# Optimization experiments

Hardware: AMD Instinct MI355X
Metric: run time of the kernel (lower is better)

The kernel has to match this reference:

```python
import jax, jax.numpy as jnp
import numpy as np
import math

# ---- module hyperparameters (from init_kwargs) ----
IN_CHANS, OUT_CHANS = 64, 64
NLAT_IN, NLON_IN = 91, 180
NLAT_OUT, NLON_OUT = 91, 180  # same resolution -> longitudinal stride 1
NR, NPHI = 5, 6               # kernel_shape
KSIZE = (NR - 1) * NPHI + 1   # 25 basis functions (1 center + (NR-1)*NPHI ring sectors)
THETA_CUTOFF = 4.0 * math.pi / float(NLAT_OUT - 1)
# latitude support window: basis vanishes for |theta_out - theta_in| > cutoff
_HALF = int(math.ceil(THETA_CUTOFF / (math.pi / (NLAT_IN - 1))))
WIN = 2 * _HALF + 1


def _precompute_psi():
    """Precompute DISCO basis tensor psi (values of the piecewise-linear
    spherical basis functions, weighted by quadrature weights), restricted to
    the latitudinal support window. Returns (psi [K,To,W,P], ti_idx [To,W])."""
    theta_in = np.pi * np.arange(NLAT_IN) / (NLAT_IN - 1)    # equiangular colatitudes
    theta_out = np.pi * np.arange(NLAT_OUT) / (NLAT_OUT - 1)
    phi_in = 2.0 * np.pi * np.arange(NLON_IN) / NLON_IN
    offs = np.arange(-_HALF, _HALF + 1)
    ti_raw = np.arange(NLAT_OUT)[:, None] + offs[None, :]    # [To, W]
    valid = (ti_raw >= 0) & (ti_raw < NLAT_IN)
    ti_idx = np.clip(ti_raw, 0, NLAT_IN - 1)
    to = theta_out[:, None, None]                            # [To,1,1]
    ti = theta_in[ti_idx][:, :, None]                        # [To,W,1]
    ph = phi_in[None, None, :]                               # [1,1,P]
    # coordinates of input point in frame where the output point (theta_out, 0)
    # is rotated to the north pole (rotation by -theta_out about y-axis)
    xx = np.cos(to) * np.sin(ti) * np.cos(ph) - np.sin(to) * np.cos(ti)
    yy = np.sin(ti) * np.sin(ph)
    zz = np.sin(to) * np.sin(ti) * np.cos(ph) + np.cos(to) * np.cos(ti)
    r = np.arccos(np.clip(zz, -1.0, 1.0))                    # great-circle distance
    phi = np.mod(np.arctan2(yy, xx), 2.0 * np.pi)            # azimuth around output point
    dr = THETA_CUTOFF / (NR - 1)
    dphi = 2.0 * np.pi / NPHI
    inside = (r <= THETA_CUTOFF) & valid[:, :, None]
    psi = np.zeros((KSIZE,) + r.shape, dtype=np.float64)
    # k = 0: isotropic center hat
    psi[0] = np.where(inside, np.maximum(0.0, 1.0 - r / dr), 0.0)
    # rings ir = 1..NR-1, azimuthal sectors ip = 0..NPHI-1 (periodic hat in phi)
    for ir in range(1, NR):
        rad = np.maximum(0.0, 1.0 - np.abs(r - ir * dr) / dr)
        for ip in range(NPHI):
            dp = np.abs(np.mod(phi - ip * dphi + np.pi, 2.0 * np.pi) - np.pi)
            ang = np.maximum(0.0, 1.0 - dp / dphi)
            psi[1 + (ir - 1) * NPHI + ip] = np.where(inside, rad * ang, 0.0)
    # fold in equiangular quadrature weights of the input grid
    quad = np.sin(theta_in) * (np.pi / (NLAT_IN - 1)) * (2.0 * np.pi / NLON_IN)
    psi = psi * quad[ti_idx][None, :, :, None]
    return jnp.asarray(psi, dtype=jnp.float32), jnp.asarray(ti_idx, dtype=jnp.int32)


PSI, TI_IDX = _precompute_psi()  # PSI: [K, To, W, P], TI_IDX: [To, W]


def setup_inputs() -> dict:
    key = jax.random.key(0)
    k1, k2 = jax.random.split(key)
    x = jax.random.normal(k1, (2, IN_CHANS, NLAT_IN, NLON_IN), dtype=jnp.float32)
    scale = 1.0 / math.sqrt(IN_CHANS * KSIZE)
    weight = scale * jax.random.normal(k2, (OUT_CHANS, IN_CHANS, KSIZE), dtype=jnp.float32)
    return {"x": x, "weight": weight}


def reference(x, weight):
    # DISCO S2 conv: out[b,o,to,q] = sum_{c,k} w[o,c,k] * sum_{ti,p} psi[k,to,ti,(p-q) mod P] * x[b,c,ti,p]
    # The longitudinal shift is a circular cross-correlation -> evaluate via rFFT.
    x = x.astype(jnp.float32)  # wrapper casts to float32 around the conv
    xw = x[:, :, TI_IDX, :]                          # [B,C,To,W,P] latitudinal gather
    Xf = jnp.fft.rfft(xw, axis=-1)                   # [B,C,To,W,F]
    Pf = jnp.fft.rfft(PSI, axis=-1)                  # [K,To,W,F]
    # correlation: FFT(z) = conj(FFT(psi)) * FFT(x), contracting the lat window
    Zf = jnp.einsum('ktwf,bctwf->bcktf', jnp.conj(Pf), Xf)   # [B,C,K,To,F]
    Of = jnp.einsum('ock,bcktf->botf', weight.astype(Zf.dtype), Zf)
    out = jnp.fft.irfft(Of, n=NLON_IN, axis=-1)      # [B,Cout,To,P]
    return out.astype(x.dtype)
```

## Files before the change

kernel.cpp:

```cpp
#include <hip/hip_runtime.h>
#include <math.h>
#include <string.h>

#define NLAT 91
#define NLON 180
#define NCH  64
#define KSZ  25
#define NW   9
#define HALF 4
#define NB   2
#define NPK  16
#define CG   8
#define PPB  (NPK / CG)
#define THREADS 192
#define EUNIT 384
#define ECAP  131072
#define UCAP  512
#define XSCAP 2560
#define LCAP  1024

#define KOFF_OFF  0
#define ROW_OFF   9472
#define UNITS_OFF 22784
#define ENTS_OFF  30976
#define BLOB_MAX  (ENTS_OFF + (size_t)ECAP * 8)

#ifndef M_PI
#define M_PI 3.14159265358979323846
#endif

typedef unsigned int u32;

static int build_tables(unsigned char* blob, int* ne_out)
{
#pragma clang fp contract(off)
    int*  koff  = (int*)(blob + KOFF_OFF);
    int4* rowi  = (int4*)(blob + ROW_OFF);
    u32*  units = (u32*)(blob + UNITS_OFF);
    u32*  ents  = (u32*)(blob + ENTS_OFF);

    static double sth[NLAT], cth[NLAT], cphv[NLON], sphv[NLON];
    for (int t = 0; t < NLAT; t++) {
        double th = (M_PI * (double)t) / 90.0;
        sth[t] = sin(th); cth[t] = cos(th);
    }
    for (int q = 0; q < NLON; q++) {
        double ph = (2.0 * M_PI * (double)q) / 180.0;
        cphv[q] = cos(ph); sphv[q] = sin(ph);
    }
    const double cutoff = (4.0 * M_PI) / 90.0;
    const double dr     = cutoff / 4.0;
    const double dphi   = (2.0 * M_PI) / 6.0;

    static int   lcnt[KSZ];
    static int   loff_[KSZ][LCAP];
    static float lval[KSZ][LCAP];

    int ne = 0, nu = 0;
    for (int t = 0; t < NLAT; t++) {
        for (int k = 0; k < KSZ; k++) lcnt[k] = 0;
        int dqmin[NW], dqmax[NW];
        for (int w = 0; w < NW; w++) { dqmin[w] = 999; dqmax[w] = -999; }
        for (int w = 0; w < NW; w++) {
            int ti_raw = t - HALF + w;
            int valid = (ti_raw >= 0) && (ti_raw < NLAT);
            int ti = ti_raw < 0 ? 0 : (ti_raw > NLAT - 1 ? NLAT - 1 : ti_raw);
            for (int dq = -89; dq <= 90; dq++) {
                int q = dq < 0 ? dq + NLON : dq;
                double t1 = sth[t] * sth[ti];
                double t2 = t1 * cphv[q];
                double t3 = cth[t] * cth[ti];
                double zz = t2 + t3;
                if (zz > 1.0) zz = 1.0;
                if (zz < -1.0) zz = -1.0;
                double r = acos(zz);
                if (!(valid && (r <= cutoff))) continue;
                if (dq < dqmin[w]) dqmin[w] = dq;
                if (dq > dqmax[w]) dqmax[w] = dq;
                double xx = (cth[t] * sth[ti]) * cphv[q] - sth[t] * cth[ti];
                double yy = sth[ti] * sphv[q];
                double phi = atan2(yy, xx);
                { double m = fmod(phi, 2.0 * M_PI); if (m < 0.0) m += 2.0 * M_PI; phi = m; }
                double quad = sth[ti] * (M_PI / 90.0) * ((2.0 * M_PI) / 180.0);
                double v0 = fmax(0.0, 1.0 - r / dr);
                float f0 = (float)(v0 * quad);
                int pid = w * 512 + (dq + 128);
                if (f0 != 0.f && lcnt[0] < LCAP) {
                    loff_[0][lcnt[0]] = pid; lval[0][lcnt[0]] = f0; lcnt[0]++;
                }
                for (int ir = 1; ir < 5; ir++) {
                    double rad = fmax(0.0, 1.0 - fabs(r - ir * dr) / dr);
                    for (int ip = 0; ip < 6; ip++) {
                        double a = (phi - ip * dphi) + M_PI;
                        double m = fmod(a, 2.0 * M_PI);
                        if (m < 0.0) m += 2.0 * M_PI;
                        double dp = fabs(m - M_PI);
                        double ang = fmax(0.0, 1.0 - dp / dphi);
                        float f = (float)((rad * ang) * quad);
                        int k = 1 + (ir - 1) * 6 + ip;
                        if (f != 0.f && lcnt[k] < LCAP) {
                            loff_[k][lcnt[k]] = pid; lval[k][lcnt[k]] = f; lcnt[k]++;
                        }
                    }
                }
            }
        }
        int rb = 0, base[NW];
        for (int w = 0; w < NW; w++) {
            int len = (dqmin[w] <= dqmax[w]) ? (NLON + dqmax[w] - dqmin[w]) : 0;
            if (rb + len > XSCAP) len = XSCAP - rb;
            int tw = t - HALF + w;
            int ti = tw < 0 ? 0 : (tw > NLAT - 1 ? NLAT - 1 : tw);
            base[w] = rb;
            rowi[t * NW + w] = make_int4(rb, len, (dqmin[w] <= dqmax[w]) ? dqmin[w] : 0, ti);
            rb += len;
        }
        int tBase = ne;
        for (int k = 0; k < KSZ; k++) {
            koff[t * (KSZ + 1) + k] = ne;
            for (int i = 0; i < lcnt[k] && ne < ECAP; i++) {
                int pid = loff_[k][i];
                int w = pid >> 9, dq = (pid & 511) - 128;
                u32 off = (u32)(base[w] + (dq - rowi[t * NW + w].z));
                ents[2 * ne] = off;
                float fv = lval[k][i];
                u32 fb; memcpy(&fb, &fv, 4);
                ents[2 * ne + 1] = fb;
                ne++;
            }
            while (((ne - koff[t * (KSZ + 1) + k]) & 3) && ne < ECAP) {
                ents[2 * ne] = 0; ents[2 * ne + 1] = 0; ne++;
            }
        }
        koff[t * (KSZ + 1) + KSZ] = ne;
        for (int e0 = tBase; e0 < ne; e0 += EUNIT) {
            int e1 = e0 + EUNIT < ne ? e0 + EUNIT : ne;
            int kb = 0;
            while (kb < KSZ &&
                   !(koff[t * (KSZ + 1) + kb] <= e0 && e0 < koff[t * (KSZ + 1) + kb + 1]))
                kb++;
            if (nu < UCAP) {
                units[nu * 4 + 0] = (u32)t;
                units[nu * 4 + 1] = (u32)e0;
                units[nu * 4 + 2] = (u32)e1;
                units[nu * 4 + 3] = (u32)kb;
                nu++;
            }
        }
    }
    *ne_out = ne;
    return nu;
}

struct GInit {
    unsigned char* blob;
    int nu, ne;
    size_t bytes;
    GInit() {
        static unsigned char storage[BLOB_MAX];
        nu = build_tables(storage, &ne);
        bytes = ENTS_OFF + (size_t)ne * 8;
        unsigned char* p = nullptr;
        if (hipHostMalloc((void**)&p, bytes) == hipSuccess && p) {
            memcpy(p, storage, bytes);
            blob = p;
        } else {
            blob = storage;
        }
    }
};
static GInit g_init;

__global__ __launch_bounds__(THREADS) void pack_x(const float* __restrict__ x,
                                                  float4* __restrict__ xp4)
{
    int t = blockIdx.x, cp = blockIdx.y, b = blockIdx.z;
    int p = threadIdx.x;
    if (p >= NLON) return;
    int c0 = cp * 4;
    float4 v;
    v.x = x[((size_t)(b * NCH + c0 + 0) * NLAT + t) * NLON + p];
    v.y = x[((size_t)(b * NCH + c0 + 1) * NLAT + t) * NLON + p];
    v.z = x[((size_t)(b * NCH + c0 + 2) * NLAT + t) * NLON + p];
    v.w = x[((size_t)(b * NCH + c0 + 3) * NLAT + t) * NLON + p];
    xp4[((size_t)(b * NPK + cp) * NLAT + t) * NLON + p] = v;
}

__global__ void pack_w(const float* __restrict__ wgt, float4* __restrict__ wt2)
{
    int i = blockIdx.x * blockDim.x + threadIdx.x;
    if (i >= NPK * KSZ * NCH) return;
    int cp = i / (KSZ * NCH);
    int rem = i - cp * (KSZ * NCH);
    int k = rem / NCH;
    int o = rem - k * NCH;
    float4 v;
    v.x = wgt[((size_t)o * NCH + cp * 4 + 0) * KSZ + k];
    v.y = wgt[((size_t)o * NCH + cp * 4 + 1) * KSZ + k];
    v.z = wgt[((size_t)o * NCH + cp * 4 + 2) * KSZ + k];
    v.w = wgt[((size_t)o * NCH + cp * 4 + 3) * KSZ + k];
    wt2[i] = v;
}

__global__ __launch_bounds__(THREADS, 3) void disco_fused(
    const float4* __restrict__ xp4, const float4* __restrict__ wt2,
    const uint2* __restrict__ ents, const int* __restrict__ koffG,
    const int4* __restrict__ rowinfoG, const uint4* __restrict__ units,
    float* __restrict__ out)
{
    uint4 uu = units[blockIdx.x];
    int t    = __builtin_amdgcn_readfirstlane((int)uu.x);
    int eBeg = __builtin_amdgcn_readfirstlane((int)uu.y);
    int eEnd = __builtin_amdgcn_readfirstlane((int)uu.z);
    int kBeg = __builtin_amdgcn_readfirstlane((int)uu.w);
    if (eBeg >= eEnd) return;
    int cg = blockIdx.y, b = blockIdx.z;
    int tid = threadIdx.x;
    int p = tid < NLON ? tid : NLON - 1;
    bool act = tid < NLON;

    __shared__ float4 xs[XSCAP];
    const int* ko = koffG + t * (KSZ + 1);
    const int4* ri9 = rowinfoG + t * NW;

    float acc[NCH];
#pragma unroll
    for (int o = 0; o < NCH; o++) acc[o] = 0.f;

    for (int pk = 0; pk < PPB; pk++) {
        int cp = cg * PPB + pk;
        __syncthreads();
#pragma unroll
        for (int w = 0; w < NW; w++) {
            int4 ri = ri9[w];
            const float4* src = xp4 + ((size_t)(b * NPK + cp) * NLAT + ri.w) * NLON;
            for (int j = tid; j < ri.y; j += THREADS) {
                int s = j + ri.z;
                if (s < 0) s += NLON;
                if (s >= NLON) s -= NLON;
                xs[ri.x + j] = src[s];
            }
        }
        __syncthreads();

        int e = eBeg, k = kBeg;
        while (e < eEnd) {
            int kend = ko[k + 1];
            if (kend > eEnd) kend = eEnd;
            if (kend > e) {
                float z00=0.f,z01=0.f,z02=0.f,z03=0.f;
                float z10=0.f,z11=0.f,z12=0.f,z13=0.f;
                float z20=0.f,z21=0.f,z22=0.f,z23=0.f;
                float z30=0.f,z31=0.f,z32=0.f,z33=0.f;
                for (; e < kend; e += 4) {
                    const uint4* e4 = (const uint4*)(ents + e);
                    uint4 A = e4[0], B = e4[1];
                    float4 x0 = xs[A.x + p];
                    float4 x1 = xs[A.z + p];
                    float4 x2 = xs[B.x + p];
                    float4 x3 = xs[B.z + p];
                    float v0 = __uint_as_float(A.y), v1 = __uint_as_float(A.w);
                    float v2 = __uint_as_float(B.y), v3 = __uint_as_float(B.w);
                    z00 = fmaf(v0, x0.x, z00); z01 = fmaf(v0, x0.y, z01);
                    z02 = fmaf(v0, x0.z, z02); z03 = fmaf(v0, x0.w, z03);
                    z10 = fmaf(v1, x1.x, z10); z11 = fmaf(v1, x1.y, z11);
                    z12 = fmaf(v1, x1.z, z12); z13 = fmaf(v1, x1.w, z13);
                    z20 = fmaf(v2, x2.x, z20); z21 = fmaf(v2, x2.y, z21);
                    z22 = fmaf(v2, x2.z, z22); z23 = fmaf(v2, x2.w, z23);
                    z30 = fmaf(v3, x3.x, z30); z31 = fmaf(v3, x3.y, z31);
                    z32 = fmaf(v3, x3.z, z32); z33 = fmaf(v3, x3.w, z33);
                }
                float zc0 = (z00 + z10) + (z20 + z30);
                float zc1 = (z01 + z11) + (z21 + z31);
                float zc2 = (z02 + z12) + (z22 + z32);
                float zc3 = (z03 + z13) + (z23 + z33);
                const float4* wk = wt2 + ((size_t)cp * KSZ + k) * NCH;
#pragma unroll
                for (int o = 0; o < NCH; o++) {
                    float4 w4 = wk[o];
                    acc[o] = fmaf(w4.w, zc3, fmaf(w4.z, zc2,
                             fmaf(w4.y, zc1, fmaf(w4.x, zc0, acc[o]))));
                }
            }
            k++;
            if (k >= KSZ) break;
        }
    }

    if (act) {
        float* op = out + ((size_t)b * NCH * NLAT * NLON) + (size_t)t * NLON + p;
#pragma unroll
        for (int o = 0; o < NCH; o++)
            atomicAdd(op + (size_t)o * (NLAT * NLON), acc[o]);
    }
}

extern "C" void kernel_launch(void* const* d_in, const int* in_sizes, int n_in,
                              void* d_out, int out_size, void* d_ws, size_t ws_size,
                              hipStream_t stream)
{
    const float* x   = (const float*)d_in[0];
    const float* wgt = (const float*)d_in[1];
    char* ws = (char*)d_ws;

    size_t cur = 0;
    auto alloc = [&](size_t bytes) { size_t o = cur; cur = (cur + bytes + 255) & ~(size_t)255; return o; };
    size_t blob_off = alloc(BLOB_MAX);
    size_t xp4_off  = alloc((size_t)NB * NPK * NLAT * NLON * 16);
    size_t wt2_off  = alloc((size_t)NPK * KSZ * NCH * 16);

    unsigned char* d_blob = (unsigned char*)(ws + blob_off);
    float4*        xp4    = (float4*)(ws + xp4_off);
    float4*        wt2    = (float4*)(ws + wt2_off);

    hipMemcpyAsync(d_blob, g_init.blob, g_init.bytes, hipMemcpyHostToDevice, stream);
    pack_x<<<dim3(NLAT, NPK, NB), THREADS, 0, stream>>>(x, xp4);
    pack_w<<<(NPK * KSZ * NCH + 255) / 256, 256, 0, stream>>>(wgt, wt2);
    hipMemsetAsync(d_out, 0, (size_t)out_size * 4, stream);

    const uint2* entsD = (const uint2*)(d_blob + ENTS_OFF);
    const int*   koffD = (const int*)(d_blob + KOFF_OFF);
    const int4*  rowD  = (const int4*)(d_blob + ROW_OFF);
    const uint4* unitD = (const uint4*)(d_blob + UNITS_OFF);

    disco_fused<<<dim3(g_init.nu, CG, NB), THREADS, 0, stream>>>(
        xp4, wt2, entsD, koffD, rowD, unitD, (float*)d_out);
}
```

Measured before the change: 407.0 us.

## Pair two entry units per block to share the staged shared-memory input tile

Each block now holds two 192-thread groups, each processing a different entry unit of the same output latitude, while they share one shared-memory load of the latitude window. Units are paired on the host, and an odd trailing unit is split in half so every pair is complete. This halves the redundant global-to-LDS staging per unit and cuts the block count, at the cost of larger blocks. Register pressure rises under the launch-bound occupancy hint of 6, and uneven work between the two halves can leave threads idle.

```diff
diff --git a/kernel.cpp b/kernel.cpp
--- a/kernel.cpp
+++ b/kernel.cpp
@@ -12,17 +12,17 @@
 #define NPK  16
 #define CG   8
 #define PPB  (NPK / CG)
-#define THREADS 192
+#define THREADS 384
 #define EUNIT 384
 #define ECAP  131072
 #define UCAP  512
-#define XSCAP 2560
+#define XSCAP 2496
 #define LCAP  1024
 
 #define KOFF_OFF  0
 #define ROW_OFF   9472
 #define UNITS_OFF 22784
-#define ENTS_OFF  30976
+#define ENTS_OFF  39168
 #define BLOB_MAX  (ENTS_OFF + (size_t)ECAP * 8)
 
 #ifndef M_PI
@@ -56,7 +56,7 @@
     static int   loff_[KSZ][LCAP];
     static float lval[KSZ][LCAP];
 
-    int ne = 0, nu = 0;
+    int ne = 0, nPairs = 0;
     for (int t = 0; t < NLAT; t++) {
         for (int k = 0; k < KSZ; k++) lcnt[k] = 0;
         int dqmin[NW], dqmax[NW];
@@ -133,23 +133,37 @@
             }
         }
         koff[t * (KSZ + 1) + KSZ] = ne;
-        for (int e0 = tBase; e0 < ne; e0 += EUNIT) {
+        int tu[128][2]; int ntu = 0;
+        for (int e0 = tBase; e0 < ne && ntu < 127; e0 += EUNIT) {
             int e1 = e0 + EUNIT < ne ? e0 + EUNIT : ne;
-            int kb = 0;
-            while (kb < KSZ &&
-                   !(koff[t * (KSZ + 1) + kb] <= e0 && e0 < koff[t * (KSZ + 1) + kb + 1]))
-                kb++;
-            if (nu < UCAP) {
-                units[nu * 4 + 0] = (u32)t;
-                units[nu * 4 + 1] = (u32)e0;
-                units[nu * 4 + 2] = (u32)e1;
-                units[nu * 4 + 3] = (u32)kb;
-                nu++;
+            tu[ntu][0] = e0; tu[ntu][1] = e1; ntu++;
+        }
+        if (ntu & 1) {
+            int a = tu[ntu - 1][0], b = tu[ntu - 1][1];
+            int m = a + (((b - a) / 2 + 3) & ~3);
+            if (m > b) m = b;
+            tu[ntu - 1][1] = m;
+            tu[ntu][0] = m; tu[ntu][1] = b;
+            ntu++;
+        }
+        for (int i = 0; i + 1 < ntu; i += 2) {
+            int kb0 = 0, kb1 = 0;
+            while (kb0 < KSZ && !(koff[t * (KSZ + 1) + kb0] <= tu[i][0] &&
+                                  tu[i][0] < koff[t * (KSZ + 1) + kb0 + 1])) kb0++;
+            while (kb1 < KSZ && !(koff[t * (KSZ + 1) + kb1] <= tu[i + 1][0] &&
+                                  tu[i + 1][0] < koff[t * (KSZ + 1) + kb1 + 1])) kb1++;
+            if (nPairs < UCAP) {
+                u32* up = units + nPairs * 8;
+                up[0] = (u32)t;
+                up[1] = (u32)tu[i][0];     up[2] = (u32)tu[i][1];     up[3] = (u32)kb0;
+                up[4] = (u32)tu[i + 1][0]; up[5] = (u32)tu[i + 1][1]; up[6] = (u32)kb1;
+                up[7] = 0;
+                nPairs++;
             }
         }
     }
     *ne_out = ne;
-    return nu;
+    return nPairs;
 }
 
 struct GInit {
@@ -171,8 +185,8 @@
 };
 static GInit g_init;
 
-__global__ __launch_bounds__(THREADS) void pack_x(const float* __restrict__ x,
-                                                  float4* __restrict__ xp4)
+__global__ __launch_bounds__(192) void pack_x(const float* __restrict__ x,
+                                              float4* __restrict__ xp4)
 {
     int t = blockIdx.x, cp = blockIdx.y, b = blockIdx.z;
     int p = threadIdx.x;
@@ -202,22 +216,25 @@
     wt2[i] = v;
 }
 
-__global__ __launch_bounds__(THREADS, 3) void disco_fused(
+__global__ __launch_bounds__(THREADS, 6) void disco_fused(
     const float4* __restrict__ xp4, const float4* __restrict__ wt2,
     const uint2* __restrict__ ents, const int* __restrict__ koffG,
     const int4* __restrict__ rowinfoG, const uint4* __restrict__ units,
     float* __restrict__ out)
 {
-    uint4 uu = units[blockIdx.x];
-    int t    = __builtin_amdgcn_readfirstlane((int)uu.x);
-    int eBeg = __builtin_amdgcn_readfirstlane((int)uu.y);
-    int eEnd = __builtin_amdgcn_readfirstlane((int)uu.z);
-    int kBeg = __builtin_amdgcn_readfirstlane((int)uu.w);
-    if (eBeg >= eEnd) return;
+    const uint4 ua = units[(size_t)blockIdx.x * 2];
+    const uint4 ub = units[(size_t)blockIdx.x * 2 + 1];
+    int tid = threadIdx.x;
+    bool grpB = (tid >= 192);
+    int t    = __builtin_amdgcn_readfirstlane((int)ua.x);
+    int eBeg = __builtin_amdgcn_readfirstlane((int)(grpB ? ub.x : ua.y));
+    int eEnd = __builtin_amdgcn_readfirstlane((int)(grpB ? ub.y : ua.z));
+    int kBeg = __builtin_amdgcn_readfirstlane((int)(grpB ? ub.z : ua.w));
     int cg = blockIdx.y, b = blockIdx.z;
-    int tid = threadIdx.x;
-    int p = tid < NLON ? tid : NLON - 1;
-    bool act = tid < NLON;
+    int lid = grpB ? tid - 192 : tid;
+    int p = lid < NLON ? lid : NLON - 1;
+    bool act = lid < NLON;
+    bool hasWork = eBeg < eEnd;
 
     __shared__ float4 xs[XSCAP];
     const int* ko = koffG + t * (KSZ + 1);
@@ -243,51 +260,53 @@
         }
         __syncthreads();
 
-        int e = eBeg, k = kBeg;
-        while (e < eEnd) {
-            int kend = ko[k + 1];
-            if (kend > eEnd) kend = eEnd;
-            if (kend > e) {
-                float z00=0.f,z01=0.f,z02=0.f,z03=0.f;
-                float z10=0.f,z11=0.f,z12=0.f,z13=0.f;
-                float z20=0.f,z21=0.f,z22=0.f,z23=0.f;
-                float z30=0.f,z31=0.f,z32=0.f,z33=0.f;
-                for (; e < kend; e += 4) {
-                    const uint4* e4 = (const uint4*)(ents + e);
-                    uint4 A = e4[0], B = e4[1];
-                    float4 x0 = xs[A.x + p];
-                    float4 x1 = xs[A.z + p];
-                    float4 x2 = xs[B.x + p];
-                    float4 x3 = xs[B.z + p];
-                    float v0 = __uint_as_float(A.y), v1 = __uint_as_float(A.w);
-                    float v2 = __uint_as_float(B.y), v3 = __uint_as_float(B.w);
-                    z00 = fmaf(v0, x0.x, z00); z01 = fmaf(v0, x0.y, z01);
-                    z02 = fmaf(v0, x0.z, z02); z03 = fmaf(v0, x0.w, z03);
-                    z10 = fmaf(v1, x1.x, z10); z11 = fmaf(v1, x1.y, z11);
-                    z12 = fmaf(v1, x1.z, z12); z13 = fmaf(v1, x1.w, z13);
-                    z20 = fmaf(v2, x2.x, z20); z21 = fmaf(v2, x2.y, z21);
-                    z22 = fmaf(v2, x2.z, z22); z23 = fmaf(v2, x2.w, z23);
-                    z30 = fmaf(v3, x3.x, z30); z31 = fmaf(v3, x3.y, z31);
-                    z32 = fmaf(v3, x3.z, z32); z33 = fmaf(v3, x3.w, z33);
+        if (hasWork) {
+            int e = eBeg, k = kBeg;
+            while (e < eEnd) {
+                int kend = ko[k + 1];
+                if (kend > eEnd) kend = eEnd;
+                if (kend > e) {
+                    float z00=0.f,z01=0.f,z02=0.f,z03=0.f;
+                    float z10=0.f,z11=0.f,z12=0.f,z13=0.f;
+                    float z20=0.f,z21=0.f,z22=0.f,z23=0.f;
+                    float z30=0.f,z31=0.f,z32=0.f,z33=0.f;
+                    for (; e < kend; e += 4) {
+                        const uint4* e4 = (const uint4*)(ents + e);
+                        uint4 A = e4[0], B = e4[1];
+                        float4 x0 = xs[A.x + p];
+                        float4 x1 = xs[A.z + p];
+                        float4 x2 = xs[B.x + p];
+                        float4 x3 = xs[B.z + p];
+                        float v0 = __uint_as_float(A.y), v1 = __uint_as_float(A.w);
+                        float v2 = __uint_as_float(B.y), v3 = __uint_as_float(B.w);
+                        z00 = fmaf(v0, x0.x, z00); z01 = fmaf(v0, x0.y, z01);
+                        z02 = fmaf(v0, x0.z, z02); z03 = fmaf(v0, x0.w, z03);
+                        z10 = fmaf(v1, x1.x, z10); z11 = fmaf(v1, x1.y, z11);
+                        z12 = fmaf(v1, x1.z, z12); z13 = fmaf(v1, x1.w, z13);
+                        z20 = fmaf(v2, x2.x, z20); z21 = fmaf(v2, x2.y, z21);
+                        z22 = fmaf(v2, x2.z, z22); z23 = fmaf(v2, x2.w, z23);
+                        z30 = fmaf(v3, x3.x, z30); z31 = fmaf(v3, x3.y, z31);
+                        z32 = fmaf(v3, x3.z, z32); z33 = fmaf(v3, x3.w, z33);
+                    }
+                    float zc0 = (z00 + z10) + (z20 + z30);
+                    float zc1 = (z01 + z11) + (z21 + z31);
+                    float zc2 = (z02 + z12) + (z22 + z32);
+                    float zc3 = (z03 + z13) + (z23 + z33);
+                    const float4* wk = wt2 + ((size_t)cp * KSZ + k) * NCH;
+#pragma unroll
+                    for (int o = 0; o < NCH; o++) {
+                        float4 w4 = wk[o];
+                        acc[o] = fmaf(w4.w, zc3, fmaf(w4.z, zc2,
+                                 fmaf(w4.y, zc1, fmaf(w4.x, zc0, acc[o]))));
+                    }
                 }
-                float zc0 = (z00 + z10) + (z20 + z30);
-                float zc1 = (z01 + z11) + (z21 + z31);
-                float zc2 = (z02 + z12) + (z22 + z32);
-                float zc3 = (z03 + z13) + (z23 + z33);
-                const float4* wk = wt2 + ((size_t)cp * KSZ + k) * NCH;
-#pragma unroll
-                for (int o = 0; o < NCH; o++) {
-                    float4 w4 = wk[o];
-                    acc[o] = fmaf(w4.w, zc3, fmaf(w4.z, zc2,
-                             fmaf(w4.y, zc1, fmaf(w4.x, zc0, acc[o]))));
-                }
-            }
-            k++;
-            if (k >= KSZ) break;
-        }
-    }
-
-    if (act) {
+                k++;
+                if (k >= KSZ) break;
+            }
+        }
+    }
+
+    if (act && hasWork) {
         float* op = out + ((size_t)b * NCH * NLAT * NLON) + (size_t)t * NLON + p;
 #pragma unroll
         for (int o = 0; o < NCH; o++)
@@ -314,7 +333,7 @@
     float4*        wt2    = (float4*)(ws + wt2_off);
 
     hipMemcpyAsync(d_blob, g_init.blob, g_init.bytes, hipMemcpyHostToDevice, stream);
-    pack_x<<<dim3(NLAT, NPK, NB), THREADS, 0, stream>>>(x, xp4);
+    pack_x<<<dim3(NLAT, NPK, NB), 192, 0, stream>>>(x, xp4);
     pack_w<<<(NPK * KSZ * NCH + 255) / 256, 256, 0, stream>>>(wgt, wt2);
     hipMemsetAsync(d_out, 0, (size_t)out_size * 4, stream);
 
```

Result: slower. 586.8 us (+44.2%).

## Group stencil points by radial/azimuthal cell to share one x load across basis functions

Applied to the files above, without the earlier changes.

Replaces the per-basis-function sparse entry list with a per-point table grouped into 30 (ring, sector) classes. Each point stores up to four hat-function weights, so one shared-memory x load feeds all basis functions that overlap it, and ring accumulators roll through the rings and flush into the output channels. The grid also changes from work units of 384 entries times 8 channel groups to one block per (latitude, channel pack, batch), dropping the unit table. In exchange, each thread holds roughly 50 extra live accumulator registers alongside the 64 output accumulators. The loop is heavily templated and unrolled, and blocks now carry uneven work per latitude.

```diff
diff --git a/kernel.cpp b/kernel.cpp
--- a/kernel.cpp
+++ b/kernel.cpp
@@ -10,20 +10,15 @@
 #define HALF 4
 #define NB   2
 #define NPK  16
-#define CG   8
-#define PPB  (NPK / CG)
 #define THREADS 192
-#define EUNIT 384
-#define ECAP  131072
-#define UCAP  512
-#define XSCAP 2560
-#define LCAP  1024
-
-#define KOFF_OFF  0
-#define ROW_OFF   9472
-#define UNITS_OFF 22784
-#define ENTS_OFF  30976
-#define BLOB_MAX  (ENTS_OFF + (size_t)ECAP * 8)
+#define XSCAP 2496
+#define PCAP  49152
+#define CCAP  2048
+
+#define CLS_OFF   0
+#define ROW_OFF   11520
+#define PSIS_OFF  24832
+#define BLOB_MAX  (PSIS_OFF + (size_t)PCAP * 16 + 64 + (size_t)PCAP * 4)
 
 #ifndef M_PI
 #define M_PI 3.14159265358979323846
@@ -31,13 +26,12 @@
 
 typedef unsigned int u32;
 
-static int build_tables(unsigned char* blob, int* ne_out)
+static int build_tables(unsigned char* blob, size_t* offs_off_out)
 {
 #pragma clang fp contract(off)
-    int*  koff  = (int*)(blob + KOFF_OFF);
-    int4* rowi  = (int4*)(blob + ROW_OFF);
-    u32*  units = (u32*)(blob + UNITS_OFF);
-    u32*  ents  = (u32*)(blob + ENTS_OFF);
+    int*   clsOff = (int*)(blob + CLS_OFF);
+    int4*  rowi   = (int4*)(blob + ROW_OFF);
+    float* psis   = (float*)(blob + PSIS_OFF);
 
     static double sth[NLAT], cth[NLAT], cphv[NLON], sphv[NLON];
     for (int t = 0; t < NLAT; t++) {
@@ -52,15 +46,18 @@
     const double dr     = cutoff / 4.0;
     const double dphi   = (2.0 * M_PI) / 6.0;
 
-    static int   lcnt[KSZ];
-    static int   loff_[KSZ][LCAP];
-    static float lval[KSZ][LCAP];
-
-    int ne = 0, nu = 0;
+    static int   cw[30][CCAP];
+    static int   cdq[30][CCAP];
+    static float cps[30][CCAP][4];
+    static int   ccnt[30];
+    static u32   toffs[PCAP];
+
+    int np = 0;
     for (int t = 0; t < NLAT; t++) {
-        for (int k = 0; k < KSZ; k++) lcnt[k] = 0;
+        for (int c = 0; c < 30; c++) ccnt[c] = 0;
         int dqmin[NW], dqmax[NW];
         for (int w = 0; w < NW; w++) { dqmin[w] = 999; dqmax[w] = -999; }
+
         for (int w = 0; w < NW; w++) {
             int ti_raw = t - HALF + w;
             int valid = (ti_raw >= 0) && (ti_raw < NLAT);
@@ -82,26 +79,51 @@
                 double phi = atan2(yy, xx);
                 { double m = fmod(phi, 2.0 * M_PI); if (m < 0.0) m += 2.0 * M_PI; phi = m; }
                 double quad = sth[ti] * (M_PI / 90.0) * ((2.0 * M_PI) / 180.0);
-                double v0 = fmax(0.0, 1.0 - r / dr);
-                float f0 = (float)(v0 * quad);
-                int pid = w * 512 + (dq + 128);
-                if (f0 != 0.f && lcnt[0] < LCAP) {
-                    loff_[0][lcnt[0]] = pid; lval[0][lcnt[0]] = f0; lcnt[0]++;
+
+                int ir = (int)floor(r / dr);  if (ir > 4) ir = 4; if (ir < 0) ir = 0;
+                int ip = (int)floor(phi / dphi); if (ip > 5) ip = 5; if (ip < 0) ip = 0;
+                int ip1 = (ip + 1) % 6;
+
+                double angL, angH;
+                {
+                    double a = (phi - ip * dphi) + M_PI;
+                    double m = fmod(a, 2.0 * M_PI); if (m < 0.0) m += 2.0 * M_PI;
+                    double dp = fabs(m - M_PI);
+                    angL = fmax(0.0, 1.0 - dp / dphi);
                 }
-                for (int ir = 1; ir < 5; ir++) {
-                    double rad = fmax(0.0, 1.0 - fabs(r - ir * dr) / dr);
-                    for (int ip = 0; ip < 6; ip++) {
-                        double a = (phi - ip * dphi) + M_PI;
-                        double m = fmod(a, 2.0 * M_PI);
-                        if (m < 0.0) m += 2.0 * M_PI;
-                        double dp = fabs(m - M_PI);
-                        double ang = fmax(0.0, 1.0 - dp / dphi);
-                        float f = (float)((rad * ang) * quad);
-                        int k = 1 + (ir - 1) * 6 + ip;
-                        if (f != 0.f && lcnt[k] < LCAP) {
-                            loff_[k][lcnt[k]] = pid; lval[k][lcnt[k]] = f; lcnt[k]++;
-                        }
-                    }
+                {
+                    double a = (phi - ip1 * dphi) + M_PI;
+                    double m = fmod(a, 2.0 * M_PI); if (m < 0.0) m += 2.0 * M_PI;
+                    double dp = fabs(m - M_PI);
+                    angH = fmax(0.0, 1.0 - dp / dphi);
+                }
+                float s0 = 0.f, s1 = 0.f, s2 = 0.f, s3 = 0.f;
+                if (ir == 0) {
+                    double rad0 = fmax(0.0, 1.0 - r / dr);
+                    double rad1 = fmax(0.0, 1.0 - fabs(r - dr) / dr);
+                    s0 = (float)(rad0 * quad);
+                    s1 = (float)((rad1 * angL) * quad);
+                    s2 = (float)((rad1 * angH) * quad);
+                } else if (ir == 4) {
+                    double rad4 = fmax(0.0, 1.0 - fabs(r - 4.0 * dr) / dr);
+                    s0 = (float)((rad4 * angL) * quad);
+                    s1 = (float)((rad4 * angH) * quad);
+                } else {
+                    double radL = fmax(0.0, 1.0 - fabs(r - ir * dr) / dr);
+                    double radH = fmax(0.0, 1.0 - fabs(r - (ir + 1) * dr) / dr);
+                    s0 = (float)((radL * angL) * quad);
+                    s1 = (float)((radL * angH) * quad);
+                    s2 = (float)((radH * angL) * quad);
+                    s3 = (float)((radH * angH) * quad);
+                }
+                if (s0 == 0.f && s1 == 0.f && s2 == 0.f && s3 == 0.f) continue;
+                int cls = ir * 6 + ip;
+                int n = ccnt[cls];
+                if (n < CCAP) {
+                    cw[cls][n] = w; cdq[cls][n] = dq;
+                    cps[cls][n][0] = s0; cps[cls][n][1] = s1;
+                    cps[cls][n][2] = s2; cps[cls][n][3] = s3;
+                    ccnt[cls] = n + 1;
                 }
             }
         }
@@ -115,51 +137,34 @@
             rowi[t * NW + w] = make_int4(rb, len, (dqmin[w] <= dqmax[w]) ? dqmin[w] : 0, ti);
             rb += len;
         }
-        int tBase = ne;
-        for (int k = 0; k < KSZ; k++) {
-            koff[t * (KSZ + 1) + k] = ne;
-            for (int i = 0; i < lcnt[k] && ne < ECAP; i++) {
-                int pid = loff_[k][i];
-                int w = pid >> 9, dq = (pid & 511) - 128;
-                u32 off = (u32)(base[w] + (dq - rowi[t * NW + w].z));
-                ents[2 * ne] = off;
-                float fv = lval[k][i];
-                u32 fb; memcpy(&fb, &fv, 4);
-                ents[2 * ne + 1] = fb;
-                ne++;
+        for (int cls = 0; cls < 30; cls++) {
+            clsOff[t * 31 + cls] = np;
+            for (int i = 0; i < ccnt[cls] && np < PCAP; i++) {
+                int w = cw[cls][i], dq = cdq[cls][i];
+                toffs[np] = (u32)(base[w] + (dq - rowi[t * NW + w].z));
+                psis[4 * np + 0] = cps[cls][i][0];
+                psis[4 * np + 1] = cps[cls][i][1];
+                psis[4 * np + 2] = cps[cls][i][2];
+                psis[4 * np + 3] = cps[cls][i][3];
+                np++;
             }
-            while (((ne - koff[t * (KSZ + 1) + k]) & 3) && ne < ECAP) {
-                ents[2 * ne] = 0; ents[2 * ne + 1] = 0; ne++;
-            }
-        }
-        koff[t * (KSZ + 1) + KSZ] = ne;
-        for (int e0 = tBase; e0 < ne; e0 += EUNIT) {
-            int e1 = e0 + EUNIT < ne ? e0 + EUNIT : ne;
-            int kb = 0;
-            while (kb < KSZ &&
-                   !(koff[t * (KSZ + 1) + kb] <= e0 && e0 < koff[t * (KSZ + 1) + kb + 1]))
-                kb++;
-            if (nu < UCAP) {
-                units[nu * 4 + 0] = (u32)t;
-                units[nu * 4 + 1] = (u32)e0;
-                units[nu * 4 + 2] = (u32)e1;
-                units[nu * 4 + 3] = (u32)kb;
-                nu++;
-            }
-        }
-    }
-    *ne_out = ne;
-    return nu;
+        }
+        clsOff[t * 31 + 30] = np;
+    }
+    size_t offs_off = (PSIS_OFF + (size_t)np * 16 + 63) & ~(size_t)63;
+    memcpy(blob + offs_off, toffs, (size_t)np * 4);
+    *offs_off_out = offs_off;
+    return np;
 }
 
 struct GInit {
     unsigned char* blob;
-    int nu, ne;
-    size_t bytes;
+    int np;
+    size_t bytes, offs_off;
     GInit() {
         static unsigned char storage[BLOB_MAX];
-        nu = build_tables(storage, &ne);
-        bytes = ENTS_OFF + (size_t)ne * 8;
+        np = build_tables(storage, &offs_off);
+        bytes = offs_off + (size_t)np * 4;
         unsigned char* p = nullptr;
         if (hipHostMalloc((void**)&p, bytes) == hipSuccess && p) {
             memcpy(p, storage, bytes);
@@ -171,8 +176,8 @@
 };
 static GInit g_init;
 
-__global__ __launch_bounds__(THREADS) void pack_x(const float* __restrict__ x,
-                                                  float4* __restrict__ xp4)
+__global__ __launch_bounds__(192) void pack_x(const float* __restrict__ x,
+                                              float4* __restrict__ xp4)
 {
     int t = blockIdx.x, cp = blockIdx.y, b = blockIdx.z;
     int p = threadIdx.x;
@@ -202,90 +207,125 @@
     wt2[i] = v;
 }
 
+template<int ROW, int IP>
+__device__ __forceinline__ void runSeg(int sBeg, int sEnd,
+    const u32* __restrict__ offsG, const float4* __restrict__ psisG,
+    const float4* xs, int p,
+    float (&z0)[4], float (&zA)[6][4], float (&zB)[6][4])
+{
+    constexpr int IP1 = (IP + 1) % 6;
+#pragma unroll 2
+    for (int s = sBeg; s < sEnd; ++s) {
+        u32 off = offsG[s];
+        float4 ps = psisG[s];
+        float4 xv = xs[off + p];
+        if (ROW == 0) {
+            z0[0] = fmaf(ps.x, xv.x, z0[0]); z0[1] = fmaf(ps.x, xv.y, z0[1]);
+            z0[2] = fmaf(ps.x, xv.z, z0[2]); z0[3] = fmaf(ps.x, xv.w, z0[3]);
+            zB[IP][0] = fmaf(ps.y, xv.x, zB[IP][0]); zB[IP][1] = fmaf(ps.y, xv.y, zB[IP][1]);
+            zB[IP][2] = fmaf(ps.y, xv.z, zB[IP][2]); zB[IP][3] = fmaf(ps.y, xv.w, zB[IP][3]);
+            zB[IP1][0] = fmaf(ps.z, xv.x, zB[IP1][0]); zB[IP1][1] = fmaf(ps.z, xv.y, zB[IP1][1]);
+            zB[IP1][2] = fmaf(ps.z, xv.z, zB[IP1][2]); zB[IP1][3] = fmaf(ps.z, xv.w, zB[IP1][3]);
+        } else if (ROW == 4) {
+            zA[IP][0] = fmaf(ps.x, xv.x, zA[IP][0]); zA[IP][1] = fmaf(ps.x, xv.y, zA[IP][1]);
+            zA[IP][2] = fmaf(ps.x, xv.z, zA[IP][2]); zA[IP][3] = fmaf(ps.x, xv.w, zA[IP][3]);
+            zA[IP1][0] = fmaf(ps.y, xv.x, zA[IP1][0]); zA[IP1][1] = fmaf(ps.y, xv.y, zA[IP1][1]);
+            zA[IP1][2] = fmaf(ps.y, xv.z, zA[IP1][2]); zA[IP1][3] = fmaf(ps.y, xv.w, zA[IP1][3]);
+        } else {
+            zA[IP][0] = fmaf(ps.x, xv.x, zA[IP][0]); zA[IP][1] = fmaf(ps.x, xv.y, zA[IP][1]);
+            zA[IP][2] = fmaf(ps.x, xv.z, zA[IP][2]); zA[IP][3] = fmaf(ps.x, xv.w, zA[IP][3]);
+            zA[IP1][0] = fmaf(ps.y, xv.x, zA[IP1][0]); zA[IP1][1] = fmaf(ps.y, xv.y, zA[IP1][1]);
+            zA[IP1][2] = fmaf(ps.y, xv.z, zA[IP1][2]); zA[IP1][3] = fmaf(ps.y, xv.w, zA[IP1][3]);
+            zB[IP][0] = fmaf(ps.z, xv.x, zB[IP][0]); zB[IP][1] = fmaf(ps.z, xv.y, zB[IP][1]);
+            zB[IP][2] = fmaf(ps.z, xv.z, zB[IP][2]); zB[IP][3] = fmaf(ps.z, xv.w, zB[IP][3]);
+            zB[IP1][0] = fmaf(ps.w, xv.x, zB[IP1][0]); zB[IP1][1] = fmaf(ps.w, xv.y, zB[IP1][1]);
+            zB[IP1][2] = fmaf(ps.w, xv.z, zB[IP1][2]); zB[IP1][3] = fmaf(ps.w, xv.w, zB[IP1][3]);
+        }
+    }
+}
+
+__device__ __forceinline__ void flushRing(float (&acc)[NCH], const float4* __restrict__ wt2cp,
+                                          int kbase, const float (&zR)[6][4])
+{
+#pragma unroll
+    for (int j = 0; j < 6; j++) {
+        const float4* wk = wt2cp + (size_t)(kbase + j) * NCH;
+#pragma unroll
+        for (int o = 0; o < NCH; o++) {
+            float4 w4 = wk[o];
+            acc[o] = fmaf(w4.w, zR[j][3], fmaf(w4.z, zR[j][2],
+                     fmaf(w4.y, zR[j][1], fmaf(w4.x, zR[j][0], acc[o]))));
+        }
+    }
+}
+
 __global__ __launch_bounds__(THREADS, 3) void disco_fused(
     const float4* __restrict__ xp4, const float4* __restrict__ wt2,
-    const uint2* __restrict__ ents, const int* __restrict__ koffG,
-    const int4* __restrict__ rowinfoG, const uint4* __restrict__ units,
+    const u32* __restrict__ offsG, const float4* __restrict__ psisG,
+    const int* __restrict__ clsOffG, const int4* __restrict__ rowG,
     float* __restrict__ out)
 {
-    uint4 uu = units[blockIdx.x];
-    int t    = __builtin_amdgcn_readfirstlane((int)uu.x);
-    int eBeg = __builtin_amdgcn_readfirstlane((int)uu.y);
-    int eEnd = __builtin_amdgcn_readfirstlane((int)uu.z);
-    int kBeg = __builtin_amdgcn_readfirstlane((int)uu.w);
-    if (eBeg >= eEnd) return;
-    int cg = blockIdx.y, b = blockIdx.z;
+    int t = blockIdx.x, cp = blockIdx.y, b = blockIdx.z;
     int tid = threadIdx.x;
     int p = tid < NLON ? tid : NLON - 1;
     bool act = tid < NLON;
 
     __shared__ float4 xs[XSCAP];
-    const int* ko = koffG + t * (KSZ + 1);
-    const int4* ri9 = rowinfoG + t * NW;
-
+#pragma unroll
+    for (int w = 0; w < NW; w++) {
+        int4 ri = rowG[t * NW + w];
+        const float4* src = xp4 + ((size_t)(b * NPK + cp) * NLAT + ri.w) * NLON;
+        for (int j = tid; j < ri.y; j += THREADS) {
+            int s = j + ri.z;
+            if (s < 0) s += NLON;
+            if (s >= NLON) s -= NLON;
+            xs[ri.x + j] = src[s];
+        }
+    }
+    __syncthreads();
+
+    const int* co = clsOffG + t * 31;
+    const float4* wt2cp = wt2 + (size_t)cp * KSZ * NCH;
+
+    float z0[4] = {0.f, 0.f, 0.f, 0.f};
+    float zA[6][4], zB[6][4];
+#pragma unroll
+    for (int j = 0; j < 6; j++)
+#pragma unroll
+        for (int c = 0; c < 4; c++) { zA[j][c] = 0.f; zB[j][c] = 0.f; }
     float acc[NCH];
 #pragma unroll
     for (int o = 0; o < NCH; o++) acc[o] = 0.f;
 
-    for (int pk = 0; pk < PPB; pk++) {
-        int cp = cg * PPB + pk;
-        __syncthreads();
-#pragma unroll
-        for (int w = 0; w < NW; w++) {
-            int4 ri = ri9[w];
-            const float4* src = xp4 + ((size_t)(b * NPK + cp) * NLAT + ri.w) * NLON;
-            for (int j = tid; j < ri.y; j += THREADS) {
-                int s = j + ri.z;
-                if (s < 0) s += NLON;
-                if (s >= NLON) s -= NLON;
-                xs[ri.x + j] = src[s];
-            }
-        }
-        __syncthreads();
-
-        int e = eBeg, k = kBeg;
-        while (e < eEnd) {
-            int kend = ko[k + 1];
-            if (kend > eEnd) kend = eEnd;
-            if (kend > e) {
-                float z00=0.f,z01=0.f,z02=0.f,z03=0.f;
-                float z10=0.f,z11=0.f,z12=0.f,z13=0.f;
-                float z20=0.f,z21=0.f,z22=0.f,z23=0.f;
-                float z30=0.f,z31=0.f,z32=0.f,z33=0.f;
-                for (; e < kend; e += 4) {
-                    const uint4* e4 = (const uint4*)(ents + e);
-                    uint4 A = e4[0], B = e4[1];
-                    float4 x0 = xs[A.x + p];
-                    float4 x1 = xs[A.z + p];
-                    float4 x2 = xs[B.x + p];
-                    float4 x3 = xs[B.z + p];
-                    float v0 = __uint_as_float(A.y), v1 = __uint_as_float(A.w);
-                    float v2 = __uint_as_float(B.y), v3 = __uint_as_float(B.w);
-                    z00 = fmaf(v0, x0.x, z00); z01 = fmaf(v0, x0.y, z01);
-                    z02 = fmaf(v0, x0.z, z02); z03 = fmaf(v0, x0.w, z03);
-                    z10 = fmaf(v1, x1.x, z10); z11 = fmaf(v1, x1.y, z11);
-                    z12 = fmaf(v1, x1.z, z12); z13 = fmaf(v1, x1.w, z13);
-                    z20 = fmaf(v2, x2.x, z20); z21 = fmaf(v2, x2.y, z21);
-                    z22 = fmaf(v2, x2.z, z22); z23 = fmaf(v2, x2.w, z23);
-                    z30 = fmaf(v3, x3.x, z30); z31 = fmaf(v3, x3.y, z31);
-                    z32 = fmaf(v3, x3.z, z32); z33 = fmaf(v3, x3.w, z33);
-                }
-                float zc0 = (z00 + z10) + (z20 + z30);
-                float zc1 = (z01 + z11) + (z21 + z31);
-                float zc2 = (z02 + z12) + (z22 + z32);
-                float zc3 = (z03 + z13) + (z23 + z33);
-                const float4* wk = wt2 + ((size_t)cp * KSZ + k) * NCH;
-#pragma unroll
-                for (int o = 0; o < NCH; o++) {
-                    float4 w4 = wk[o];
-                    acc[o] = fmaf(w4.w, zc3, fmaf(w4.z, zc2,
-                             fmaf(w4.y, zc1, fmaf(w4.x, zc0, acc[o]))));
-                }
-            }
-            k++;
-            if (k >= KSZ) break;
-        }
-    }
+#define SEG(ROW, IP) runSeg<ROW, IP>(co[(ROW)*6+(IP)], co[(ROW)*6+(IP)+1], \
+                                     offsG, psisG, xs, p, z0, zA, zB)
+#define ROW6(ROW) SEG(ROW,0); SEG(ROW,1); SEG(ROW,2); SEG(ROW,3); SEG(ROW,4); SEG(ROW,5)
+#define ROLL() { _Pragma("unroll") for (int j = 0; j < 6; j++) { \
+                 _Pragma("unroll") for (int c = 0; c < 4; c++) { \
+                   zA[j][c] = zB[j][c]; zB[j][c] = 0.f; } } }
+
+    ROW6(0);
+    {
+        const float4* wk = wt2cp;
+#pragma unroll
+        for (int o = 0; o < NCH; o++) {
+            float4 w4 = wk[o];
+            acc[o] = fmaf(w4.w, z0[3], fmaf(w4.z, z0[2],
+                     fmaf(w4.y, z0[1], fmaf(w4.x, z0[0], acc[o]))));
+        }
+    }
+    ROLL();
+    ROW6(1);
+    flushRing(acc, wt2cp, 1, zA);
+    ROLL();
+    ROW6(2);
+    flushRing(acc, wt2cp, 7, zA);
+    ROLL();
+    ROW6(3);
+    flushRing(acc, wt2cp, 13, zA);
+    ROLL();
+    ROW6(4);
+    flushRing(acc, wt2cp, 19, zA);
 
     if (act) {
         float* op = out + ((size_t)b * NCH * NLAT * NLON) + (size_t)t * NLON + p;
@@ -314,15 +354,15 @@
     float4*        wt2    = (float4*)(ws + wt2_off);
 
     hipMemcpyAsync(d_blob, g_init.blob, g_init.bytes, hipMemcpyHostToDevice, stream);
-    pack_x<<<dim3(NLAT, NPK, NB), THREADS, 0, stream>>>(x, xp4);
+    pack_x<<<dim3(NLAT, NPK, NB), 192, 0, stream>>>(x, xp4);
     pack_w<<<(NPK * KSZ * NCH + 255) / 256, 256, 0, stream>>>(wgt, wt2);
     hipMemsetAsync(d_out, 0, (size_t)out_size * 4, stream);
 
-    const uint2* entsD = (const uint2*)(d_blob + ENTS_OFF);
-    const int*   koffD = (const int*)(d_blob + KOFF_OFF);
-    const int4*  rowD  = (const int4*)(d_blob + ROW_OFF);
-    const uint4* unitD = (const uint4*)(d_blob + UNITS_OFF);
-
-    disco_fused<<<dim3(g_init.nu, CG, NB), THREADS, 0, stream>>>(
-        xp4, wt2, entsD, koffD, rowD, unitD, (float*)d_out);
-}
+    const u32*    offsD = (const u32*)(d_blob + g_init.offs_off);
+    const float4* psisD = (const float4*)(d_blob + PSIS_OFF);
+    const int*    clsD  = (const int*)(d_blob + CLS_OFF);
+    const int4*   rowD  = (const int4*)(d_blob + ROW_OFF);
+
+    disco_fused<<<dim3(NLAT, NPK, NB), THREADS, 0, stream>>>(
+        xp4, wt2, offsD, psisD, clsD, rowD, (float*)d_out);
+}
```

Result: slower. 577.9 us (+42.0%).
